# Kernel optimization log

Measured on AMD Instinct MI355X. Metric: run time of the kernel, lower is better.

The kernel has to match this reference:

```python
import jax, jax.numpy as jnp
import numpy as np

CH = 8        # CHANNELS
CONVS = 8     # CONVOLUTIONS
HID = 32      # HIDDEN
NTYPES = 6    # NODE_TYPES
N_NODES = 200000
N_EDGES = 6400000
ENTRIES = 2048
BN_EPS = 1e-5


def setup_inputs() -> dict:
    key = jax.random.key(0)
    ks = jax.random.split(key, 12)
    x = jax.random.randint(ks[0], (N_NODES,), 0, NTYPES)
    edge_index = jax.random.randint(ks[1], (2, N_EDGES), 0, N_NODES)
    entry_index = jax.random.randint(ks[2], (ENTRIES,), 0, N_NODES)
    emb = jax.random.normal(ks[3], (NTYPES, CH), jnp.float32)
    bn_gamma = jnp.ones((CONVS, CH), jnp.float32)
    bn_beta = jnp.zeros((CONVS, CH), jnp.float32)
    conv_w = jax.random.normal(ks[4], (CONVS, CH, CH), jnp.float32) * (1.0 / np.sqrt(CH))
    conv_b = jnp.zeros((CONVS, CH), jnp.float32)
    hidden_w = jax.random.normal(ks[5], (2 * CH, HID), jnp.float32) * (1.0 / np.sqrt(2 * CH))
    hidden_b = jnp.zeros((HID,), jnp.float32)
    out_w = jax.random.normal(ks[6], (HID, 1), jnp.float32) * (1.0 / np.sqrt(HID))
    out_b = jnp.zeros((1,), jnp.float32)
    return dict(x=x, edge_index=edge_index, entry_index=entry_index, emb=emb,
                bn_gamma=bn_gamma, bn_beta=bn_beta, conv_w=conv_w, conv_b=conv_b,
                hidden_w=hidden_w, hidden_b=hidden_b, out_w=out_w, out_b=out_b)


def reference(x, edge_index, entry_index, emb, bn_gamma, bn_beta,
              conv_w, conv_b, hidden_w, hidden_b, out_w, out_b):
    N = x.shape[0]
    src, dst = edge_index[0], edge_index[1]
    # GCN symmetric normalization with self-loops (PyG gcn_norm):
    # deg[i] = 1 (self loop) + in-degree(i); norm_e = deg[src]^-1/2 * deg[dst]^-1/2
    deg = jax.ops.segment_sum(jnp.ones(src.shape[0], jnp.float32), dst, num_segments=N) + 1.0
    dinv = jax.lax.rsqrt(deg)                       # [N]
    enorm = (dinv[src] * dinv[dst])[:, None]        # [E,1]
    self_norm = (dinv * dinv)[:, None]              # [N,1] self-loop coefficient

    h = emb[x]                                      # [N,CH]
    for l in range(CONVS):
        # BatchNorm (training mode: batch statistics over nodes)
        mu = h.mean(axis=0)
        var = jnp.mean((h - mu) ** 2, axis=0)
        hn = (h - mu) * jax.lax.rsqrt(var + BN_EPS) * bn_gamma[l] + bn_beta[l]
        # GCNConv: linear transform then normalized aggregation
        ht = hn @ conv_w[l]                         # [N,CH]
        agg = jax.ops.segment_sum(ht[src] * enorm, dst, num_segments=N)
        agg = agg + ht * self_norm + conv_b[l]
        h = jax.nn.relu(h + agg)                    # residual + ReLU

    xe = h[entry_index]                             # [E,CH]
    E = xe.shape[0]
    # cartesian_prod(line, line): pair[i,j] = concat(xe[i], xe[j])
    pair = jnp.concatenate([
        jnp.broadcast_to(xe[:, None, :], (E, E, CH)),
        jnp.broadcast_to(xe[None, :, :], (E, E, CH)),
    ], axis=-1)                                     # [E,E,2CH]
    hid = jax.nn.relu(pair @ hidden_w + hidden_b)   # [E,E,HID]
    out = (hid @ out_w + out_b).reshape(E, E)
    return out
```

## Files before the change

### kernel.cpp

```cpp
#include <hip/hip_runtime.h>
#include <hip/hip_fp16.h>

#define NNODES 200000
#define NEDGES 6400000
#define NENT   2048
#define CH     8
#define HID    32
#define NCONV  8
#define BN_EPS 1e-5f

#define BSZ    196
#define NBUCK  1024
#define SRCB   391
#define CHUNK  4096
#define NCHUNK ((NEDGES + CHUNK - 1) / CHUNK)
#define SPAD   16
#define SCOP   16
#define SUBCAP 8192
#define ESTG   512
#define ACCS   9

#define I16SCALE  2048.0f
#define I16INV    (1.0f/2048.0f)

#define SSLOT  (2*CH*SCOP*SPAD)

__device__ __forceinline__ int bucket_of(int d){ return (int)((unsigned)d / 196u); }

__device__ __forceinline__ int xcd_swz(int bid, int nwg){
  int xcd = bid & 7, idx = bid >> 3;
  int q = nwg >> 3, r = nwg & 7;
  return (xcd < r ? xcd*(q+1) : r*(q+1) + (xcd-r)*q) + idx;
}

__global__ __launch_bounds__(256) void k_chist(const int* __restrict__ dst, int* __restrict__ cnt, int E){
  __shared__ int hist[NBUCK];
  for(int t=threadIdx.x; t<NBUCK; t+=256) hist[t]=0;
  __syncthreads();
  int e0 = blockIdx.x*CHUNK;
  int n = min(CHUNK, E-e0);
  for(int i=threadIdx.x; i<n; i+=256) atomicAdd(&hist[bucket_of(dst[e0+i])], 1);
  __syncthreads();
  for(int t=threadIdx.x; t<NBUCK; t+=256) cnt[(size_t)blockIdx.x*NBUCK + t] = hist[t];
}

__global__ __launch_bounds__(256) void k_cscan(int* __restrict__ cnt, int* __restrict__ total){
  int b = xcd_swz(blockIdx.x, NBUCK);
  __shared__ int sd[256];
  int carry = 0;
  for(int base=0; base<NCHUNK; base+=256){
    int c = base + threadIdx.x;
    int v = (c<NCHUNK) ? cnt[(size_t)c*NBUCK + b] : 0;
    sd[threadIdx.x] = v; __syncthreads();
    #pragma unroll
    for(int o=1; o<256; o<<=1){
      int x = (threadIdx.x>=o) ? sd[threadIdx.x-o] : 0;
      __syncthreads();
      sd[threadIdx.x] += x;
      __syncthreads();
    }
    if(c<NCHUNK) cnt[(size_t)c*NBUCK + b] = carry + sd[threadIdx.x] - v;
    carry += sd[255];
    __syncthreads();
  }
  if(threadIdx.x==0) total[b] = carry;
}

__global__ __launch_bounds__(1024) void k_bscan(const int* __restrict__ total, int* __restrict__ bbase){
  __shared__ int sd[1024];
  int t = threadIdx.x;
  int v = total[t];
  sd[t] = v; __syncthreads();
  #pragma unroll
  for(int o=1; o<1024; o<<=1){
    int x = (t>=o) ? sd[t-o] : 0;
    __syncthreads();
    sd[t] += x;
    __syncthreads();
  }
  bbase[t] = sd[t] - v;
  if(t==1023) bbase[NBUCK] = sd[1023];
}

__global__ __launch_bounds__(1024) void k_bin(const int* __restrict__ src, const int* __restrict__ dst,
                                              const int* __restrict__ cnt, const int* __restrict__ total,
                                              const int* __restrict__ bbase,
                                              unsigned int* __restrict__ binned, int E){
  __shared__ int excl[NBUCK], cur[NBUCK], base[NBUCK];
  __shared__ unsigned int pin[CHUNK];
  __shared__ unsigned short bk_in[CHUNK];
  __shared__ unsigned int sorted[CHUNK];
  __shared__ unsigned short sbkt[CHUNK];
  __shared__ int sd[1024];
  int c = xcd_swz(blockIdx.x, NCHUNK);
  int e0 = c*CHUNK, n = min(CHUNK, E-e0);
  int t = threadIdx.x;
  for(int i=t; i<n; i+=1024){
    int s = src[e0+i], d = dst[e0+i];
    int b = bucket_of(d);
    pin[i]   = ((unsigned)(d - b*BSZ)<<18) | (unsigned)s;
    bk_in[i] = (unsigned short)b;
  }
  int h0 = cnt[(size_t)c*NBUCK + t];
  int h1 = (c+1 < NCHUNK) ? cnt[(size_t)(c+1)*NBUCK + t] : total[t];
  int hv = h1 - h0;
  sd[t] = hv; __syncthreads();
  #pragma unroll
  for(int o=1; o<1024; o<<=1){
    int x = (t>=o) ? sd[t-o] : 0;
    __syncthreads();
    sd[t] += x;
    __syncthreads();
  }
  {
    int ex = sd[t] - hv;
    excl[t] = ex; cur[t] = ex;
    base[t] = bbase[t] + h0;
  }
  __syncthreads();
  for(int i=t; i<n; i+=1024){
    int b = bk_in[i];
    int slot = atomicAdd(&cur[b], 1);
    sorted[slot] = pin[i];
    sbkt[slot]   = (unsigned short)b;
  }
  __syncthreads();
  for(int i=t; i<n; i+=1024){
    int b = sbkt[i];
    binned[ base[b] + (i - excl[b]) ] = sorted[i];
  }
}

__global__ __launch_bounds__(512) void k_sub(const unsigned int* __restrict__ binned,
                                             const int* __restrict__ bbase,
                                             unsigned int* __restrict__ binned2,
                                             float* __restrict__ dinv, int N){
  __shared__ int hd[BSZ];
  __shared__ int hs[SRCB];
  __shared__ int cur[SRCB];
  __shared__ int sd[512];
  __shared__ unsigned int stage[SUBCAP];
  int b = blockIdx.x;
  int t = threadIdx.x;
  if(t < BSZ)  hd[t] = 0;
  if(t < SRCB) hs[t] = 0;
  __syncthreads();
  int s0 = bbase[b], s1 = bbase[b+1];
  for(int i=s0+t; i<s1; i+=512){
    unsigned p = binned[i];
    atomicAdd(&hd[p>>18], 1);
    atomicAdd(&hs[(p & 0x3FFFF)>>9], 1);
  }
  __syncthreads();
  if(t < BSZ){
    int node = b*BSZ + t;
    if(node < N) dinv[node] = 1.0f / sqrtf((float)hd[t] + 1.0f);
  }
  int hv = (t<SRCB) ? hs[t] : 0;
  sd[t] = hv; __syncthreads();
  #pragma unroll
  for(int o=1; o<512; o<<=1){
    int x = (t>=o) ? sd[t-o] : 0;
    __syncthreads();
    sd[t] += x;
    __syncthreads();
  }
  if(t<SRCB) cur[t] = sd[t] - hv;
  __syncthreads();
  int len = s1 - s0;
  if(len <= SUBCAP){
    for(int i=s0+t; i<s1; i+=512){
      unsigned p = binned[i];
      int slot = atomicAdd(&cur[(p & 0x3FFFF)>>9], 1);
      stage[slot] = p;
    }
    __syncthreads();
    for(int i=t; i<len; i+=512) binned2[s0 + i] = stage[i];
  } else {
    for(int i=s0+t; i<s1; i+=512){
      unsigned p = binned[i];
      int slot = atomicAdd(&cur[(p & 0x3FFFF)>>9], 1);
      binned2[s0 + slot] = p;
    }
  }
}

__global__ __launch_bounds__(256) void k_init_h(const int* __restrict__ x, const float* __restrict__ emb,
                                                float* __restrict__ h, float* __restrict__ stats0, int N){
  int i = blockIdx.x*256 + threadIdx.x;
  float v[CH];
  #pragma unroll
  for(int c=0;c<CH;c++) v[c]=0.f;
  if(i < N){
    int tt = x[i];
    const float4* ep = (const float4*)(emb + (size_t)tt*CH);
    float4 a = ep[0], b = ep[1];
    float4* hp = (float4*)(h + (size_t)i*CH);
    hp[0] = a; hp[1] = b;
    v[0]=a.x; v[1]=a.y; v[2]=a.z; v[3]=a.w; v[4]=b.x; v[5]=b.y; v[6]=b.z; v[7]=b.w;
  }
  float s[CH], q[CH];
  #pragma unroll
  for(int c=0;c<CH;c++){ s[c]=v[c]; q[c]=v[c]*v[c]; }
  #pragma unroll
  for(int off=32; off>0; off>>=1){
    #pragma unroll
    for(int c=0;c<CH;c++){ s[c]+=__shfl_down(s[c],off); q[c]+=__shfl_down(q[c],off); }
  }
  __shared__ float ls[4][2*CH];
  int wave = threadIdx.x>>6, lane = threadIdx.x&63;
  if(lane==0){
    #pragma unroll
    for(int c=0;c<CH;c++){ ls[wave][c]=s[c]; ls[wave][CH+c]=q[c]; }
  }
  __syncthreads();
  if(threadIdx.x < 2*CH){
    float tsum = ls[0][threadIdx.x]+ls[1][threadIdx.x]+ls[2][threadIdx.x]+ls[3][threadIdx.x];
    unsafeAtomicAdd(&stats0[(threadIdx.x*SCOP + (blockIdx.x & (SCOP-1)))*SPAD], tsum);
  }
}

__global__ __launch_bounds__(256) void k_ht(const float* __restrict__ h, const float* __restrict__ stats_l,
                                            const float* __restrict__ gamma, const float* __restrict__ beta,
                                            const float* __restrict__ convw,
                                            const float* __restrict__ dinv,
                                            short* __restrict__ hts, int l, int N){
  __shared__ float A[CH*CH], c0[CH], sA[CH], sT[CH];
  int t = threadIdx.x;
  if(t < CH){
    float mu = 0.f, ex2 = 0.f;
    #pragma unroll
    for(int c=0;c<SCOP;c++){
      mu  += stats_l[((t   )*SCOP + c)*SPAD];
      ex2 += stats_l[((CH+t)*SCOP + c)*SPAD];
    }
    const float invN = 1.0f / (float)NNODES;
    mu *= invN; ex2 *= invN;
    float var = ex2 - mu*mu;
    float r   = 1.0f / sqrtf(var + BN_EPS);
    float sc  = r * gamma[l*CH+t];
    sA[t] = sc;
    sT[t] = beta[l*CH+t] - mu*sc;
  }
  __syncthreads();
  if(t < CH*CH){
    int ci = t>>3, co = t&7;
    A[t] = sA[ci] * convw[(l*CH+ci)*CH+co];
  }
  if(t < CH){
    float a = 0.f;
    #pragma unroll
    for(int ci=0;ci<CH;ci++) a += sT[ci]*convw[(l*CH+ci)*CH+t];
    c0[t] = a;
  }
  __syncthreads();
  int i = blockIdx.x*blockDim.x + threadIdx.x;
  if(i >= N) return;
  const float4* hp = (const float4*)(h + (size_t)i*CH);
  float4 a = hp[0], b = hp[1];
  float v[CH] = {a.x,a.y,a.z,a.w,b.x,b.y,b.z,b.w};
  float o[CH];
  #pragma unroll
  for(int co=0;co<CH;co++) o[co]=c0[co];
  #pragma unroll
  for(int ci=0;ci<CH;ci++){
    float vv = v[ci];
    #pragma unroll
    for(int co=0;co<CH;co++) o[co] += vv*A[ci*CH+co];
  }
  float dn = dinv[i] * I16SCALE;
  union { short ss[CH]; uint4 u; } pk;
  #pragma unroll
  for(int c=0;c<CH;c++){
    float val = fminf(fmaxf(o[c]*dn, -32767.f), 32767.f);
    pk.ss[c] = (short)__float2int_rn(val);
  }
  *(uint4*)(hts + (size_t)i*CH) = pk.u;
}

__global__ __launch_bounds__(512) void k_push(const unsigned int* __restrict__ binned2,
                                              const int* __restrict__ bbase,
                                              const short* __restrict__ hts,
                                              const float* __restrict__ dinv,
                                              const float* __restrict__ convb,
                                              float* __restrict__ h, float* __restrict__ stats_next,
                                              int l, int N){
  __shared__ int acc[BSZ*ACCS];
  __shared__ unsigned est[ESTG];
  int b = blockIdx.x, t = threadIdx.x;
  for(int i=t; i<BSZ*ACCS; i+=512) acc[i] = 0;
  __syncthreads();
  int s0 = bbase[b], s1 = bbase[b+1];
  int lane8 = t & 7;
  int g = t >> 3;
  for(int off = s0; off < s1; off += ESTG){
    int n = min(ESTG, s1 - off);
    if(t < n) est[t] = binned2[off + t];
    __syncthreads();
    for(int e = g*4; e < n; e += 256){
      int m = n - e;
      if(m >= 4){
        unsigned p0 = est[e], p1 = est[e+1], p2 = est[e+2], p3 = est[e+3];
        int v0 = (int)hts[(size_t)(p0 & 0x3FFFF)*CH + lane8];
        int v1 = (int)hts[(size_t)(p1 & 0x3FFFF)*CH + lane8];
        int v2 = (int)hts[(size_t)(p2 & 0x3FFFF)*CH + lane8];
        int v3 = (int)hts[(size_t)(p3 & 0x3FFFF)*CH + lane8];
        atomicAdd(&acc[(p0>>18)*ACCS + lane8], v0);
        atomicAdd(&acc[(p1>>18)*ACCS + lane8], v1);
        atomicAdd(&acc[(p2>>18)*ACCS + lane8], v2);
        atomicAdd(&acc[(p3>>18)*ACCS + lane8], v3);
      } else {
        for(int i=0; i<m; i++){
          unsigned p = est[e+i];
          int v = (int)hts[(size_t)(p & 0x3FFFF)*CH + lane8];
          atomicAdd(&acc[(p>>18)*ACCS + lane8], v);
        }
      }
    }
    __syncthreads();
  }
  float vv[CH];
  #pragma unroll
  for(int c=0;c<CH;c++) vv[c]=0.f;
  int node = b*BSZ + t;
  if(t < BSZ && node < N){
    float av[CH];
    #pragma unroll
    for(int c=0;c<CH;c++) av[c] = (float)acc[t*ACCS + c] * I16INV;
    union { short ss[CH]; uint4 u; } su;
    su.u = *(const uint4*)(hts + (size_t)node*CH);
    const float4* hp = (const float4*)(h + (size_t)node*CH);
    float4 h0 = hp[0], h1 = hp[1];
    float hv2[CH] = {h0.x,h0.y,h0.z,h0.w,h1.x,h1.y,h1.z,h1.w};
    float dn = dinv[node];
    #pragma unroll
    for(int c=0;c<CH;c++){
      float sv = (float)su.ss[c] * I16INV;
      float r = hv2[c] + convb[l*CH + c] + dn*(av[c] + sv);
      vv[c] = fmaxf(r, 0.f);
    }
    float4* hw4 = (float4*)(h + (size_t)node*CH);
    hw4[0] = make_float4(vv[0],vv[1],vv[2],vv[3]);
    hw4[1] = make_float4(vv[4],vv[5],vv[6],vv[7]);
  }
  float s[CH], q[CH];
  #pragma unroll
  for(int c=0;c<CH;c++){ s[c]=vv[c]; q[c]=vv[c]*vv[c]; }
  #pragma unroll
  for(int off=32; off>0; off>>=1){
    #pragma unroll
    for(int c=0;c<CH;c++){ s[c]+=__shfl_down(s[c],off); q[c]+=__shfl_down(q[c],off); }
  }
  __shared__ float ls[8][2*CH];
  int wave = t>>6, lane = t&63;
  if(lane==0){
    #pragma unroll
    for(int c=0;c<CH;c++){ ls[wave][c]=s[c]; ls[wave][CH+c]=q[c]; }
  }
  __syncthreads();
  if(t < 2*CH){
    float tot = 0.f;
    #pragma unroll
    for(int w=0; w<8; w++) tot += ls[w][t];
    unsafeAtomicAdd(&stats_next[(t*SCOP + (b & (SCOP-1)))*SPAD], tot);
  }
}

__global__ __launch_bounds__(256) void k_uv(const int* __restrict__ entry, const float* __restrict__ h,
                                            const float* __restrict__ hw, const float* __restrict__ hb,
                                            float* __restrict__ u, float* __restrict__ v){
  __shared__ float w[2*CH*HID];
  __shared__ float b[HID];
  for(int t=threadIdx.x; t<2*CH*HID; t+=256) w[t]=hw[t];
  if(threadIdx.x<HID) b[threadIdx.x]=hb[threadIdx.x];
  __syncthreads();
  int k = blockIdx.x*blockDim.x + threadIdx.x;
  if(k >= NENT) return;
  int node = entry[k];
  const float4* hp = (const float4*)(h + (size_t)node*CH);
  float4 a = hp[0], b4 = hp[1];
  float xe[CH] = {a.x,a.y,a.z,a.w,b4.x,b4.y,b4.z,b4.w};
  #pragma unroll 4
  for(int c=0;c<HID;c++){
    float uu = 0.f, vv = b[c];
    #pragma unroll
    for(int ci=0;ci<CH;ci++){
      uu += xe[ci]*w[ci*HID+c];
      vv += xe[ci]*w[(CH+ci)*HID+c];
    }
    u[(size_t)k*HID+c] = uu;
    v[(size_t)k*HID+c] = vv;
  }
}

__global__ __launch_bounds__(256) void k_pair(const float* __restrict__ u, const float* __restrict__ v,
                                              const float* __restrict__ ow, const float* __restrict__ ob,
                                              float* __restrict__ out){
  __shared__ float us[16][HID+1];
  __shared__ float vs[64][HID+1];
  __shared__ float wo[HID];
  int tid = threadIdx.x;
  int jb = blockIdx.x*64, ib = blockIdx.y*16;
  for(int t=tid; t<16*HID; t+=256) us[t>>5][t&31] = u[(size_t)(ib + (t>>5))*HID + (t&31)];
  for(int t=tid; t<64*HID; t+=256) vs[t>>5][t&31] = v[(size_t)(jb + (t>>5))*HID + (t&31)];
  if(tid<HID) wo[tid]=ow[tid];
  __syncthreads();
  int tx = tid&63, ty = tid>>6;
  float a0=0.f, a1=0.f, a2=0.f, a3=0.f;
  #pragma unroll
  for(int c=0;c<HID;c++){
    float vv = vs[tx][c];
    float w  = wo[c];
    a0 += fmaxf(us[ty   ][c]+vv, 0.f)*w;
    a1 += fmaxf(us[ty+4 ][c]+vv, 0.f)*w;
    a2 += fmaxf(us[ty+8 ][c]+vv, 0.f)*w;
    a3 += fmaxf(us[ty+12][c]+vv, 0.f)*w;
  }
  float o0 = ob[0];
  size_t base = (size_t)ib*2048 + jb + tx;
  out[base + (size_t)(ty   )*2048] = a0+o0;
  out[base + (size_t)(ty+4 )*2048] = a1+o0;
  out[base + (size_t)(ty+8 )*2048] = a2+o0;
  out[base + (size_t)(ty+12)*2048] = a3+o0;
}

extern "C" void kernel_launch(void* const* d_in, const int* in_sizes, int n_in,
                              void* d_out, int out_size, void* d_ws, size_t ws_size,
                              hipStream_t stream){
  const int*   x     = (const int*)d_in[0];
  const int*   ei    = (const int*)d_in[1];
  const int*   entry = (const int*)d_in[2];
  const float* emb   = (const float*)d_in[3];
  const float* gamma = (const float*)d_in[4];
  const float* beta  = (const float*)d_in[5];
  const float* convw = (const float*)d_in[6];
  const float* convb = (const float*)d_in[7];
  const float* hw    = (const float*)d_in[8];
  const float* hb    = (const float*)d_in[9];
  const float* ow    = (const float*)d_in[10];
  const float* ob    = (const float*)d_in[11];
  const int* srcp = ei;
  const int* dstp = ei + NEDGES;

  char* ws = (char*)d_ws;
  size_t o = 0;
  auto alloc = [&](size_t bytes){ void* p = ws + o; o += (bytes + 255) & ~(size_t)255; return p; };
  int*      cnt    = (int*)     alloc((size_t)NCHUNK*NBUCK*4);
  int*      total  = (int*)     alloc(NBUCK*4);
  int*      bbase  = (int*)     alloc((NBUCK+1)*4);
  unsigned* binned = (unsigned*)alloc((size_t)NEDGES*4);
  unsigned* binned2= (unsigned*)alloc((size_t)NEDGES*4);
  float*    dinv   = (float*)   alloc(NNODES*4);
  float*    h      = (float*)   alloc((size_t)NNODES*CH*4);
  short*    hts    = (short*)   alloc((size_t)NNODES*CH*2);
  float*    stats  = (float*)   alloc((size_t)(NCONV+1)*SSLOT*4);
  float*    ub     = (float*)   alloc((size_t)NENT*HID*4);
  float*    vb     = (float*)   alloc((size_t)NENT*HID*4);
  (void)ws_size; (void)in_sizes; (void)n_in; (void)out_size;

  k_chist<<<NCHUNK, 256, 0, stream>>>(dstp, cnt, NEDGES);
  k_cscan<<<NBUCK, 256, 0, stream>>>(cnt, total);
  k_bscan<<<1, 1024, 0, stream>>>(total, bbase);
  k_bin  <<<NCHUNK, 1024, 0, stream>>>(srcp, dstp, cnt, total, bbase, binned, NEDGES);
  k_sub  <<<NBUCK, 512, 0, stream>>>(binned, bbase, binned2, dinv, NNODES);

  hipMemsetAsync(stats, 0, (size_t)(NCONV+1)*SSLOT*sizeof(float), stream);
  k_init_h<<<(NNODES+255)/256, 256, 0, stream>>>(x, emb, h, stats, NNODES);

  for(int l=0; l<NCONV; l++){
    k_ht  <<<(NNODES+255)/256, 256, 0, stream>>>(h, stats + (size_t)l*SSLOT, gamma, beta, convw,
                                                 dinv, hts, l, NNODES);
    k_push<<<NBUCK, 512, 0, stream>>>(binned2, bbase, hts, dinv, convb, h,
                                      stats + (size_t)(l+1)*SSLOT, l, NNODES);
  }

  k_uv<<<NENT/256, 256, 0, stream>>>(entry, h, hw, hb, ub, vb);
  dim3 pg(2048/64, 2048/16);
  k_pair<<<pg, 256, 0, stream>>>(ub, vb, ow, ob, (float*)d_out);
}
```

Measured before the change: 470.5 us.

## Pack two biased int16 channels per 64-bit LDS atomic in GCN push

```diff
diff --git a/kernel.cpp b/kernel.cpp
--- a/kernel.cpp
+++ b/kernel.cpp
@@ -18,10 +18,10 @@
 #define SCOP   16
 #define SUBCAP 8192
 #define ESTG   512
-#define ACCS   9
 
 #define I16SCALE  2048.0f
 #define I16INV    (1.0f/2048.0f)
+#define BIAS      32768
 
 #define SSLOT  (2*CH*SCOP*SPAD)
 
@@ -224,7 +224,7 @@
                                             const float* __restrict__ gamma, const float* __restrict__ beta,
                                             const float* __restrict__ convw,
                                             const float* __restrict__ dinv,
-                                            short* __restrict__ hts, int l, int N){
+                                            unsigned* __restrict__ hts32, int l, int N){
   __shared__ float A[CH*CH], c0[CH], sA[CH], sT[CH];
   int t = threadIdx.x;
   if(t < CH){
@@ -269,52 +269,59 @@
     for(int co=0;co<CH;co++) o[co] += vv*A[ci*CH+co];
   }
   float dn = dinv[i] * I16SCALE;
-  union { short ss[CH]; uint4 u; } pk;
-  #pragma unroll
-  for(int c=0;c<CH;c++){
-    float val = fminf(fmaxf(o[c]*dn, -32767.f), 32767.f);
-    pk.ss[c] = (short)__float2int_rn(val);
-  }
-  *(uint4*)(hts + (size_t)i*CH) = pk.u;
+  unsigned pk[4];
+  #pragma unroll
+  for(int j=0;j<4;j++){
+    float f0 = fminf(fmaxf(o[2*j  ]*dn, -32767.f), 32767.f);
+    float f1 = fminf(fmaxf(o[2*j+1]*dn, -32767.f), 32767.f);
+    unsigned u0 = (unsigned)(__float2int_rn(f0) + BIAS);
+    unsigned u1 = (unsigned)(__float2int_rn(f1) + BIAS);
+    pk[j] = u0 | (u1 << 16);
+  }
+  *(uint4*)(hts32 + (size_t)i*4) = make_uint4(pk[0],pk[1],pk[2],pk[3]);
 }
 
 __global__ __launch_bounds__(512) void k_push(const unsigned int* __restrict__ binned2,
                                               const int* __restrict__ bbase,
-                                              const short* __restrict__ hts,
+                                              const unsigned* __restrict__ hts32,
                                               const float* __restrict__ dinv,
                                               const float* __restrict__ convb,
                                               float* __restrict__ h, float* __restrict__ stats_next,
                                               int l, int N){
-  __shared__ int acc[BSZ*ACCS];
+  __shared__ unsigned long long acc[BSZ*4];
   __shared__ unsigned est[ESTG];
   int b = blockIdx.x, t = threadIdx.x;
-  for(int i=t; i<BSZ*ACCS; i+=512) acc[i] = 0;
+  for(int i=t; i<BSZ*4; i+=512) acc[i] = 0ull;
   __syncthreads();
   int s0 = bbase[b], s1 = bbase[b+1];
-  int lane8 = t & 7;
-  int g = t >> 3;
+  int lane4 = t & 3;
+  int g = t >> 2;
+  int e0 = g*4;
   for(int off = s0; off < s1; off += ESTG){
     int n = min(ESTG, s1 - off);
     if(t < n) est[t] = binned2[off + t];
     __syncthreads();
-    for(int e = g*4; e < n; e += 256){
-      int m = n - e;
-      if(m >= 4){
-        unsigned p0 = est[e], p1 = est[e+1], p2 = est[e+2], p3 = est[e+3];
-        int v0 = (int)hts[(size_t)(p0 & 0x3FFFF)*CH + lane8];
-        int v1 = (int)hts[(size_t)(p1 & 0x3FFFF)*CH + lane8];
-        int v2 = (int)hts[(size_t)(p2 & 0x3FFFF)*CH + lane8];
-        int v3 = (int)hts[(size_t)(p3 & 0x3FFFF)*CH + lane8];
-        atomicAdd(&acc[(p0>>18)*ACCS + lane8], v0);
-        atomicAdd(&acc[(p1>>18)*ACCS + lane8], v1);
-        atomicAdd(&acc[(p2>>18)*ACCS + lane8], v2);
-        atomicAdd(&acc[(p3>>18)*ACCS + lane8], v3);
-      } else {
-        for(int i=0; i<m; i++){
-          unsigned p = est[e+i];
-          int v = (int)hts[(size_t)(p & 0x3FFFF)*CH + lane8];
-          atomicAdd(&acc[(p>>18)*ACCS + lane8], v);
-        }
+    int m = n - e0;
+    if(m >= 4){
+      unsigned p0=est[e0], p1=est[e0+1], p2=est[e0+2], p3=est[e0+3];
+      unsigned w0 = hts32[(size_t)(p0 & 0x3FFFF)*4 + lane4];
+      unsigned w1 = hts32[(size_t)(p1 & 0x3FFFF)*4 + lane4];
+      unsigned w2 = hts32[(size_t)(p2 & 0x3FFFF)*4 + lane4];
+      unsigned w3 = hts32[(size_t)(p3 & 0x3FFFF)*4 + lane4];
+      unsigned long long v0 = (unsigned long long)(w0 & 0xFFFFu) | ((unsigned long long)(w0 >> 16) << 32);
+      unsigned long long v1 = (unsigned long long)(w1 & 0xFFFFu) | ((unsigned long long)(w1 >> 16) << 32);
+      unsigned long long v2 = (unsigned long long)(w2 & 0xFFFFu) | ((unsigned long long)(w2 >> 16) << 32);
+      unsigned long long v3 = (unsigned long long)(w3 & 0xFFFFu) | ((unsigned long long)(w3 >> 16) << 32);
+      atomicAdd(&acc[(p0>>18)*4 + lane4], v0);
+      atomicAdd(&acc[(p1>>18)*4 + lane4], v1);
+      atomicAdd(&acc[(p2>>18)*4 + lane4], v2);
+      atomicAdd(&acc[(p3>>18)*4 + lane4], v3);
+    } else if(m > 0){
+      for(int i=0; i<m; i++){
+        unsigned p = est[e0+i];
+        unsigned w = hts32[(size_t)(p & 0x3FFFF)*4 + lane4];
+        unsigned long long v = (unsigned long long)(w & 0xFFFFu) | ((unsigned long long)(w >> 16) << 32);
+        atomicAdd(&acc[(p>>18)*4 + lane4], v);
       }
     }
     __syncthreads();
@@ -324,20 +331,31 @@
   for(int c=0;c<CH;c++) vv[c]=0.f;
   int node = b*BSZ + t;
   if(t < BSZ && node < N){
+    float dn = dinv[node];
+    int deg = (int)roundf(1.0f/(dn*dn)) - 1;
+    int bias = deg * BIAS;
     float av[CH];
     #pragma unroll
-    for(int c=0;c<CH;c++) av[c] = (float)acc[t*ACCS + c] * I16INV;
-    union { short ss[CH]; uint4 u; } su;
-    su.u = *(const uint4*)(hts + (size_t)node*CH);
+    for(int j=0;j<4;j++){
+      unsigned long long a = acc[t*4 + j];
+      int lo = (int)(unsigned)(a & 0xFFFFFFFFull) - bias;
+      int hi = (int)(unsigned)(a >> 32)           - bias;
+      av[2*j]   = (float)lo * I16INV;
+      av[2*j+1] = (float)hi * I16INV;
+    }
+    uint4 su = *(const uint4*)(hts32 + (size_t)node*4);
+    unsigned sw[4] = {su.x, su.y, su.z, su.w};
     const float4* hp = (const float4*)(h + (size_t)node*CH);
     float4 h0 = hp[0], h1 = hp[1];
     float hv2[CH] = {h0.x,h0.y,h0.z,h0.w,h1.x,h1.y,h1.z,h1.w};
-    float dn = dinv[node];
-    #pragma unroll
-    for(int c=0;c<CH;c++){
-      float sv = (float)su.ss[c] * I16INV;
-      float r = hv2[c] + convb[l*CH + c] + dn*(av[c] + sv);
-      vv[c] = fmaxf(r, 0.f);
+    #pragma unroll
+    for(int j=0;j<4;j++){
+      float sv0 = (float)((int)(sw[j] & 0xFFFFu) - BIAS) * I16INV;
+      float sv1 = (float)((int)(sw[j] >> 16)     - BIAS) * I16INV;
+      float r0 = hv2[2*j]   + convb[l*CH + 2*j]   + dn*(av[2*j]   + sv0);
+      float r1 = hv2[2*j+1] + convb[l*CH + 2*j+1] + dn*(av[2*j+1] + sv1);
+      vv[2*j]   = fmaxf(r0, 0.f);
+      vv[2*j+1] = fmaxf(r1, 0.f);
     }
     float4* hw4 = (float4*)(h + (size_t)node*CH);
     hw4[0] = make_float4(vv[0],vv[1],vv[2],vv[3]);
@@ -452,7 +470,7 @@
   unsigned* binned2= (unsigned*)alloc((size_t)NEDGES*4);
   float*    dinv   = (float*)   alloc(NNODES*4);
   float*    h      = (float*)   alloc((size_t)NNODES*CH*4);
-  short*    hts    = (short*)   alloc((size_t)NNODES*CH*2);
+  unsigned* hts32  = (unsigned*)alloc((size_t)NNODES*4*4);
   float*    stats  = (float*)   alloc((size_t)(NCONV+1)*SSLOT*4);
   float*    ub     = (float*)   alloc((size_t)NENT*HID*4);
   float*    vb     = (float*)   alloc((size_t)NENT*HID*4);
@@ -469,8 +487,8 @@
 
   for(int l=0; l<NCONV; l++){
     k_ht  <<<(NNODES+255)/256, 256, 0, stream>>>(h, stats + (size_t)l*SSLOT, gamma, beta, convw,
-                                                 dinv, hts, l, NNODES);
-    k_push<<<NBUCK, 512, 0, stream>>>(binned2, bbase, hts, dinv, convb, h,
+                                                 dinv, hts32, l, NNODES);
+    k_push<<<NBUCK, 512, 0, stream>>>(binned2, bbase, hts32, dinv, convb, h,
                                       stats + (size_t)(l+1)*SSLOT, l, NNODES);
   }
 
```

Measured after the change: 467.6 us. No clear change (-0.6%).
